# Kernel tuning notes

Measured on AMD Instinct MI355X. Metric: run time of the kernel, lower is better.

## Reference

```python
import jax, jax.numpy as jnp
import numpy as np
from jax import lax

NUM_GROUPS = 16
POOL_KS = 2
CLAMP_MIN = 0.0
CLAMP_MAX = 1.0
EPS = 1e-5


def setup_inputs() -> dict:
    key = jax.random.key(0)
    k1, k2, k3, k4, k5 = jax.random.split(key, 5)
    B, Cin, H, W = 32, 64, 128, 128
    Cout, K = 128, 3
    x = jax.random.normal(k1, (B, Cin, H, W), dtype=jnp.float32)
    fan_in = Cin * K * K
    bound = 1.0 / np.sqrt(fan_in)
    conv_w = jax.random.uniform(k2, (Cout, Cin, K, K), jnp.float32, -bound, bound)
    conv_b = jax.random.uniform(k3, (Cout,), jnp.float32, -bound, bound)
    gn_w = jnp.ones((Cout,), jnp.float32)
    gn_b = jnp.zeros((Cout,), jnp.float32)
    scale = jnp.ones((Cout, 1, 1), jnp.float32)
    return {"x": x, "conv_w": conv_w, "conv_b": conv_b,
            "gn_w": gn_w, "gn_b": gn_b, "scale": scale}


def reference(x, conv_w, conv_b, gn_w, gn_b, scale):
    # Conv2d, stride=1, padding=0  -> (B, Cout, Ho, Wo)
    y = lax.conv_general_dilated(
        x, conv_w, window_strides=(1, 1), padding="VALID",
        dimension_numbers=("NCHW", "OIHW", "NCHW"))
    y = y + conv_b[None, :, None, None]
    B, C, H, W = y.shape
    G = NUM_GROUPS
    # GroupNorm (biased variance, as in torch)
    yg = y.reshape(B, G, C // G, H, W)
    mean = jnp.mean(yg, axis=(2, 3, 4), keepdims=True)
    var = jnp.mean(jnp.square(yg), axis=(2, 3, 4), keepdims=True) - jnp.square(mean)
    yn = (yg - mean) * lax.rsqrt(var + EPS)
    yn = yn.reshape(B, C, H, W) * gn_w[None, :, None, None] + gn_b[None, :, None, None]
    # per-channel scale
    yn = yn * scale[None, :, :, :]
    # MaxPool2d(kernel=POOL_KS, stride=POOL_KS), VALID
    pooled = lax.reduce_window(
        yn, -jnp.inf, lax.max,
        window_dimensions=(1, 1, POOL_KS, POOL_KS),
        window_strides=(1, 1, POOL_KS, POOL_KS),
        padding="VALID")
    return jnp.clip(pooled, CLAMP_MIN, CLAMP_MAX)
```

## Files before the change

kernel.cpp:

```cpp
#include <hip/hip_runtime.h>
#include <stdint.h>
#include <stddef.h>

#define HIN 128
#define WIN 128
#define CINC 64
#define COUTC 128
#define HO 126
#define WO 126
#define HP 63
#define WP 63
#define NB 32
#define NG 16

typedef __bf16 bf16x8 __attribute__((ext_vector_type(8)));
typedef float f32x16 __attribute__((ext_vector_type(16)));

__device__ __forceinline__ unsigned int f2bf(float f) {
  unsigned int u = __float_as_uint(f);
  return (u + 0x7fffu + ((u >> 16) & 1u)) >> 16;
}

__global__ __launch_bounds__(256) void wtrans_k(const float* __restrict__ w,
                                                unsigned short* __restrict__ wt2) {
  int i = blockIdx.x * 256 + threadIdx.x;
  if (i >= 73728) return;
  int j = i & 7;
  int co = (i >> 3) & 127;
  int th = i >> 10;
  int half = th & 1, ks = (th >> 1) & 3, tap = th >> 3;
  int kh = tap / 3, kw = tap - 3 * kh;
  int cin = ks * 16 + half * 8 + j;
  float v = w[((co * CINC + cin) * 3 + kh) * 3 + kw];
  wt2[i] = (unsigned short)f2bf(v);
}

__global__ __launch_bounds__(256, 4) void conv_k(const float* __restrict__ x,
                                                 const unsigned short* __restrict__ wt2,
                                                 const float* __restrict__ conv_b,
                                                 float* __restrict__ out,
                                                 float* __restrict__ stats) {
  __shared__ __align__(16) unsigned int x_lds[10 * 18 * 32];

  int t = threadIdx.x;
  int owb = blockIdx.x & 7, ohb = blockIdx.x >> 3;
  int b = blockIdx.y;
  int oh0 = ohb * 8, ow0 = owb * 16;

  const float* xb = x + (size_t)b * CINC * HIN * WIN;
  for (int i = t; i < 1600; i += 256) {
    int c4 = i % 5;
    int j = i / 5;
    int p = j & 31;
    int r = j >> 5;
    int gr = oh0 + r;
    int gc0 = ow0 + c4 * 4;
    float4 v0 = make_float4(0.f, 0.f, 0.f, 0.f);
    float4 v1 = v0;
    if (gr < HIN && gc0 < WIN) {
      const float* base = xb + ((size_t)(2 * p) * HIN + gr) * WIN + gc0;
      v0 = *(const float4*)base;
      v1 = *(const float4*)(base + HIN * WIN);
    }
    float e0[4] = {v0.x, v0.y, v0.z, v0.w};
    float e1[4] = {v1.x, v1.y, v1.z, v1.w};
#pragma unroll
    for (int cc = 0; cc < 4; ++cc) {
      int c = c4 * 4 + cc;
      if (c < 18) {
        unsigned int d = f2bf(e0[cc]) | (f2bf(e1[cc]) << 16);
        x_lds[(r * 18 + c) * 32 + (p ^ ((c & 7) << 2))] = d;
      }
    }
  }
  __syncthreads();

  int lane = t & 63, wave = t >> 6;
  int half = lane >> 5, m = lane & 31;
  int n0 = wave * 32, co = n0 + m;
  float bias = conv_b[co];
  f32x16 acc[4];
#pragma unroll
  for (int mt = 0; mt < 4; ++mt)
#pragma unroll
    for (int r = 0; r < 16; ++r) acc[mt][r] = bias;

  const unsigned short* wb = wt2 + (half * 1024 + co * 8);
  int pr0 = m >> 4, pc0 = m & 15;

#pragma unroll
  for (int kh = 0; kh < 3; ++kh)
#pragma unroll
    for (int kw = 0; kw < 3; ++kw) {
      int tap = kh * 3 + kw;
      int c = pc0 + kw;
      int swz = (c & 7) << 2;
      int rcb = ((pr0 + kh) * 18 + c) * 32;
#pragma unroll
      for (int ks = 0; ks < 4; ++ks) {
        bf16x8 bfr = __builtin_bit_cast(
            bf16x8, *(const uint4*)(wb + (tap * 4 + ks) * 2048));
        int ab = rcb + ((ks * 8 + half * 4) ^ swz);
#pragma unroll
        for (int mt = 0; mt < 4; ++mt) {
          bf16x8 afr = __builtin_bit_cast(bf16x8, *(const uint4*)&x_lds[ab + mt * 1152]);
          acc[mt] = __builtin_amdgcn_mfma_f32_32x32x16_bf16(afr, bfr, acc[mt], 0, 0, 0);
        }
      }
    }

  float s = 0.f, qs = 0.f;
  float* ob = out + (size_t)(b * COUTC + co) * HP * WP;
#pragma unroll
  for (int mt = 0; mt < 4; ++mt) {
#pragma unroll
    for (int reg = 0; reg < 16; ++reg) {
      int c16 = (reg & 3) + 4 * half + 8 * ((reg >> 2) & 1);
      int r8 = mt * 2 + (reg >> 3);
      if ((oh0 + r8) < HO && (ow0 + c16) < WO) {
        float v = acc[mt][reg];
        s += v;
        qs += v * v;
      }
    }
    int oh2 = ohb * 4 + mt;
    if (oh2 < HP) {
#pragma unroll
      for (int i = 0; i < 4; ++i) {
        int r0 = 2 * i;
        int ow2 = owb * 8 + (i & 1) + 2 * half + 4 * (i >> 1);
        if (ow2 < WP) {
          float mx = fmaxf(fmaxf(acc[mt][r0], acc[mt][r0 + 1]),
                           fmaxf(acc[mt][r0 + 8], acc[mt][r0 + 9]));
          ob[oh2 * WP + ow2] = mx;
        }
      }
    }
  }

#pragma unroll
  for (int off = 4; off; off >>= 1) {
    s += __shfl_down(s, off, 8);
    qs += __shfl_down(qs, off, 8);
  }
  if ((lane & 7) == 0) {
    int g = co >> 3;
    atomicAdd(&stats[(b * NG + g) * 2 + 0], s);
    atomicAdd(&stats[(b * NG + g) * 2 + 1], qs);
  }
}

__global__ __launch_bounds__(256) void fin_k(float* __restrict__ out,
                                             const float* __restrict__ stats,
                                             const float* __restrict__ gn_w,
                                             const float* __restrict__ gn_b,
                                             const float* __restrict__ scale) {
  int idx = blockIdx.x * 256 + threadIdx.x;
  int bc = idx / (HP * WP);
  int c = bc & 127, b = bc >> 7;
  int g = c >> 3;
  float su = stats[(b * NG + g) * 2 + 0];
  float sq = stats[(b * NG + g) * 2 + 1];
  const float inv_cnt = 1.0f / (8.0f * HO * WO);
  float mean = su * inv_cnt;
  float var = fmaxf(sq * inv_cnt - mean * mean, 0.f);
  float rstd = rsqrtf(var + 1e-5f);
  float A = rstd * gn_w[c] * scale[c];
  float B = (gn_b[c] - mean * rstd * gn_w[c]) * scale[c];
  float v = out[idx];
  out[idx] = fminf(fmaxf(fmaf(v, A, B), 0.0f), 1.0f);
}

extern "C" void kernel_launch(void* const* d_in, const int* in_sizes, int n_in,
                              void* d_out, int out_size, void* d_ws, size_t ws_size,
                              hipStream_t stream) {
  const float* x      = (const float*)d_in[0];
  const float* conv_w = (const float*)d_in[1];
  const float* conv_b = (const float*)d_in[2];
  const float* gn_w   = (const float*)d_in[3];
  const float* gn_b   = (const float*)d_in[4];
  const float* scale  = (const float*)d_in[5];
  float* out = (float*)d_out;

  float* stats        = (float*)d_ws;
  unsigned short* wt2 = (unsigned short*)((char*)d_ws + 4096);

  hipMemsetAsync(d_ws, 0, 4096, stream);
  wtrans_k<<<288, 256, 0, stream>>>(conv_w, wt2);

  conv_k<<<dim3(128, NB), 256, 0, stream>>>(x, wt2, conv_b, out, stats);

  fin_k<<<63504, 256, 0, stream>>>(out, stats, gn_w, gn_b, scale);
}
```

Before: 391.3 us.

## Enlarge conv tile to 16x16 with waves split over rows, vectorize finalize

Each conv block now covers a 16x16 output tile with all 128 output channels. Every wave handles 4 output rows and 4 channel tiles, so each A fragment loaded from LDS is reused across 4 weight fragments and each weight fragment across 2 row tiles. This halves the number of blocks and the halo overhead of the input staging. The cost is more LDS, more accumulator registers and lower occupancy (launch bounds go from 4 to 2). The finalize kernel now uses a grid-stride loop over float4 elements to cut the launch count and issue wider memory accesses.

```diff
diff --git a/kernel.cpp b/kernel.cpp
--- a/kernel.cpp
+++ b/kernel.cpp
@@ -35,20 +35,20 @@
   wt2[i] = (unsigned short)f2bf(v);
 }
 
-__global__ __launch_bounds__(256, 4) void conv_k(const float* __restrict__ x,
+__global__ __launch_bounds__(256, 2) void conv_k(const float* __restrict__ x,
                                                  const unsigned short* __restrict__ wt2,
                                                  const float* __restrict__ conv_b,
                                                  float* __restrict__ out,
                                                  float* __restrict__ stats) {
-  __shared__ __align__(16) unsigned int x_lds[10 * 18 * 32];
+  __shared__ __align__(16) unsigned int x_lds[18 * 18 * 32];
 
   int t = threadIdx.x;
-  int owb = blockIdx.x & 7, ohb = blockIdx.x >> 3;
+  int tw = blockIdx.x & 7, th = blockIdx.x >> 3;
   int b = blockIdx.y;
-  int oh0 = ohb * 8, ow0 = owb * 16;
+  int oh0 = th * 16, ow0 = tw * 16;
 
   const float* xb = x + (size_t)b * CINC * HIN * WIN;
-  for (int i = t; i < 1600; i += 256) {
+  for (int i = t; i < 2880; i += 256) {
     int c4 = i % 5;
     int j = i / 5;
     int p = j & 31;
@@ -77,76 +77,96 @@
 
   int lane = t & 63, wave = t >> 6;
   int half = lane >> 5, m = lane & 31;
-  int n0 = wave * 32, co = n0 + m;
-  float bias = conv_b[co];
-  f32x16 acc[4];
-#pragma unroll
-  for (int mt = 0; mt < 4; ++mt)
-#pragma unroll
-    for (int r = 0; r < 16; ++r) acc[mt][r] = bias;
-
-  const unsigned short* wb = wt2 + (half * 1024 + co * 8);
-  int pr0 = m >> 4, pc0 = m & 15;
+  f32x16 acc[2][4];
+#pragma unroll
+  for (int nt = 0; nt < 4; ++nt) {
+    float bias = conv_b[nt * 32 + m];
+#pragma unroll
+    for (int mt = 0; mt < 2; ++mt)
+#pragma unroll
+      for (int r = 0; r < 16; ++r) acc[mt][nt][r] = bias;
+  }
+
+  const unsigned short* wb = wt2 + half * 1024 + m * 8;
+  int prb = wave * 4 + (m >> 4);
+  int pc = m & 15;
 
 #pragma unroll
   for (int kh = 0; kh < 3; ++kh)
 #pragma unroll
     for (int kw = 0; kw < 3; ++kw) {
       int tap = kh * 3 + kw;
-      int c = pc0 + kw;
+      int c = pc + kw;
       int swz = (c & 7) << 2;
-      int rcb = ((pr0 + kh) * 18 + c) * 32;
 #pragma unroll
       for (int ks = 0; ks < 4; ++ks) {
-        bf16x8 bfr = __builtin_bit_cast(
-            bf16x8, *(const uint4*)(wb + (tap * 4 + ks) * 2048));
-        int ab = rcb + ((ks * 8 + half * 4) ^ swz);
-#pragma unroll
-        for (int mt = 0; mt < 4; ++mt) {
-          bf16x8 afr = __builtin_bit_cast(bf16x8, *(const uint4*)&x_lds[ab + mt * 1152]);
-          acc[mt] = __builtin_amdgcn_mfma_f32_32x32x16_bf16(afr, bfr, acc[mt], 0, 0, 0);
+        int ab = c * 32 + ((ks * 8 + half * 4) ^ swz);
+        bf16x8 afr[2];
+#pragma unroll
+        for (int mt = 0; mt < 2; ++mt)
+          afr[mt] = __builtin_bit_cast(
+              bf16x8, *(const uint4*)&x_lds[(prb + mt * 2 + kh) * (18 * 32) + ab]);
+        const unsigned short* wk = wb + (tap * 4 + ks) * 2048;
+#pragma unroll
+        for (int nt = 0; nt < 4; ++nt) {
+          bf16x8 bfr = __builtin_bit_cast(bf16x8, *(const uint4*)(wk + nt * 256));
+#pragma unroll
+          for (int mt = 0; mt < 2; ++mt)
+            acc[mt][nt] = __builtin_amdgcn_mfma_f32_32x32x16_bf16(afr[mt], bfr,
+                                                                  acc[mt][nt], 0, 0, 0);
         }
       }
     }
 
-  float s = 0.f, qs = 0.f;
-  float* ob = out + (size_t)(b * COUTC + co) * HP * WP;
-#pragma unroll
-  for (int mt = 0; mt < 4; ++mt) {
-#pragma unroll
-    for (int reg = 0; reg < 16; ++reg) {
-      int c16 = (reg & 3) + 4 * half + 8 * ((reg >> 2) & 1);
-      int r8 = mt * 2 + (reg >> 3);
-      if ((oh0 + r8) < HO && (ow0 + c16) < WO) {
-        float v = acc[mt][reg];
-        s += v;
-        qs += v * v;
-      }
-    }
-    int oh2 = ohb * 4 + mt;
-    if (oh2 < HP) {
-#pragma unroll
-      for (int i = 0; i < 4; ++i) {
-        int r0 = 2 * i;
-        int ow2 = owb * 8 + (i & 1) + 2 * half + 4 * (i >> 1);
-        if (ow2 < WP) {
-          float mx = fmaxf(fmaxf(acc[mt][r0], acc[mt][r0 + 1]),
-                           fmaxf(acc[mt][r0 + 8], acc[mt][r0 + 9]));
-          ob[oh2 * WP + ow2] = mx;
+  float s[4] = {0.f, 0.f, 0.f, 0.f}, qs[4] = {0.f, 0.f, 0.f, 0.f};
+#pragma unroll
+  for (int nt = 0; nt < 4; ++nt) {
+    int co = nt * 32 + m;
+    float* ob = out + (size_t)(b * COUTC + co) * (HP * WP);
+#pragma unroll
+    for (int mt = 0; mt < 2; ++mt) {
+#pragma unroll
+      for (int reg = 0; reg < 16; ++reg) {
+        int c16 = (reg & 3) + 4 * half + 8 * ((reg >> 2) & 1);
+        int r8 = wave * 4 + mt * 2 + (reg >> 3);
+        if ((oh0 + r8) < HO && (ow0 + c16) < WO) {
+          float v = acc[mt][nt][reg];
+          s[nt] += v;
+          qs[nt] += v * v;
         }
       }
-    }
-  }
-
-#pragma unroll
-  for (int off = 4; off; off >>= 1) {
-    s += __shfl_down(s, off, 8);
-    qs += __shfl_down(qs, off, 8);
-  }
-  if ((lane & 7) == 0) {
-    int g = co >> 3;
-    atomicAdd(&stats[(b * NG + g) * 2 + 0], s);
-    atomicAdd(&stats[(b * NG + g) * 2 + 1], qs);
+      int oh2 = th * 8 + wave * 2 + mt;
+      if (oh2 < HP) {
+#pragma unroll
+        for (int i = 0; i < 4; ++i) {
+          int r0 = 2 * i;
+          int ow2 = tw * 8 + (i & 1) + 2 * half + 4 * (i >> 1);
+          if (ow2 < WP) {
+            float mx = fmaxf(fmaxf(acc[mt][nt][r0], acc[mt][nt][r0 + 1]),
+                             fmaxf(acc[mt][nt][r0 + 8], acc[mt][nt][r0 + 9]));
+            ob[oh2 * WP + ow2] = mx;
+          }
+        }
+      }
+    }
+  }
+
+#pragma unroll
+  for (int nt = 0; nt < 4; ++nt) {
+    float sv = s[nt], qv = qs[nt];
+    sv += __shfl_xor(sv, 32);
+    qv += __shfl_xor(qv, 32);
+    sv += __shfl_down(sv, 4, 8);
+    qv += __shfl_down(qv, 4, 8);
+    sv += __shfl_down(sv, 2, 8);
+    qv += __shfl_down(qv, 2, 8);
+    sv += __shfl_down(sv, 1, 8);
+    qv += __shfl_down(qv, 1, 8);
+    if (half == 0 && (m & 7) == 0) {
+      int g = nt * 4 + (m >> 3);
+      atomicAdd(&stats[(b * NG + g) * 2 + 0], sv);
+      atomicAdd(&stats[(b * NG + g) * 2 + 1], qv);
+    }
   }
 }
 
@@ -155,20 +175,30 @@
                                              const float* __restrict__ gn_w,
                                              const float* __restrict__ gn_b,
                                              const float* __restrict__ scale) {
-  int idx = blockIdx.x * 256 + threadIdx.x;
-  int bc = idx / (HP * WP);
-  int c = bc & 127, b = bc >> 7;
-  int g = c >> 3;
-  float su = stats[(b * NG + g) * 2 + 0];
-  float sq = stats[(b * NG + g) * 2 + 1];
+  const int total4 = NB * COUTC * HP * WP / 4;
   const float inv_cnt = 1.0f / (8.0f * HO * WO);
-  float mean = su * inv_cnt;
-  float var = fmaxf(sq * inv_cnt - mean * mean, 0.f);
-  float rstd = rsqrtf(var + 1e-5f);
-  float A = rstd * gn_w[c] * scale[c];
-  float B = (gn_b[c] - mean * rstd * gn_w[c]) * scale[c];
-  float v = out[idx];
-  out[idx] = fminf(fmaxf(fmaf(v, A, B), 0.0f), 1.0f);
+  int stride = gridDim.x * 256;
+  for (int i4 = blockIdx.x * 256 + threadIdx.x; i4 < total4; i4 += stride) {
+    float4 v = ((const float4*)out)[i4];
+    float r[4] = {v.x, v.y, v.z, v.w};
+    int idx0 = i4 * 4;
+#pragma unroll
+    for (int e = 0; e < 4; ++e) {
+      int idx = idx0 + e;
+      int bc = idx / (HP * WP);
+      int c = bc & 127, b = bc >> 7;
+      int g = c >> 3;
+      float su = stats[(b * NG + g) * 2 + 0];
+      float sq = stats[(b * NG + g) * 2 + 1];
+      float mean = su * inv_cnt;
+      float var = fmaxf(sq * inv_cnt - mean * mean, 0.f);
+      float rstd = rsqrtf(var + 1e-5f);
+      float A = rstd * gn_w[c] * scale[c];
+      float B = (gn_b[c] - mean * rstd * gn_w[c]) * scale[c];
+      r[e] = fminf(fmaxf(fmaf(r[e], A, B), 0.0f), 1.0f);
+    }
+    ((float4*)out)[i4] = make_float4(r[0], r[1], r[2], r[3]);
+  }
 }
 
 extern "C" void kernel_launch(void* const* d_in, const int* in_sizes, int n_in,
@@ -188,7 +218,7 @@
   hipMemsetAsync(d_ws, 0, 4096, stream);
   wtrans_k<<<288, 256, 0, stream>>>(conv_w, wt2);
 
-  conv_k<<<dim3(128, NB), 256, 0, stream>>>(x, wt2, conv_b, out, stats);
-
-  fin_k<<<63504, 256, 0, stream>>>(out, stats, gn_w, gn_b, scale);
-}
+  conv_k<<<dim3(64, NB), 256, 0, stream>>>(x, wt2, conv_b, out, stats);
+
+  fin_k<<<4096, 256, 0, stream>>>(out, stats, gn_w, gn_b, scale);
+}
```

New measurement: 502.4 us. 28.4% more time.
